# Performance work log

Measured on AMD Instinct MI355X. Metric: run time of the kernel, lower is better.

## Reference

```python
import jax, jax.numpy as jnp
import numpy as np

N_NODES = 65536
N_EDGES = 1048576
IN_DIM = 96
HID = 128
OUT = 2 * HID  # GATv2 out_channels (heads=1, concat)
N_ACT = 20
EDGE_DIM = 3
NEG_SLOPE = 0.2
LN_EPS = 1e-5


def _glorot(key, shape):
    fan_in, fan_out = shape[0], shape[1]
    lim = float(np.sqrt(6.0 / (fan_in + fan_out)))
    return jax.random.uniform(key, shape, jnp.float32, -lim, lim)


def setup_inputs() -> dict:
    key = jax.random.key(0)
    ks = jax.random.split(key, 16)
    inputs = jax.random.normal(ks[0], (N_NODES, IN_DIM), jnp.float32)
    edge_index = jax.random.randint(ks[1], (2, N_EDGES), 0, N_NODES, jnp.int32)
    edge_attr = jax.random.normal(ks[2], (N_EDGES, EDGE_DIM), jnp.float32)
    return {
        "inputs": inputs,
        "edge_index": edge_index,
        "edge_attr": edge_attr,
        # MLP base (n_layers=2, layer_norm=True)
        "W0": _glorot(ks[3], (IN_DIM, HID)), "b0": jnp.zeros((HID,), jnp.float32),
        "g0": jnp.ones((HID,), jnp.float32), "be0": jnp.zeros((HID,), jnp.float32),
        "W1": _glorot(ks[4], (HID, HID)), "b1": jnp.zeros((HID,), jnp.float32),
        "g1": jnp.ones((HID,), jnp.float32), "be1": jnp.zeros((HID,), jnp.float32),
        # GATv2Conv params (heads=1)
        "Wl": _glorot(ks[5], (HID, OUT)), "bl": jnp.zeros((OUT,), jnp.float32),
        "Wr": _glorot(ks[6], (HID, OUT)), "br": jnp.zeros((OUT,), jnp.float32),
        "We": _glorot(ks[7], (EDGE_DIM, OUT)),
        "att": _glorot(ks[8], (OUT, 1))[:, 0],
        "Wres": _glorot(ks[9], (HID, OUT)),
        "gat_bias": jnp.zeros((OUT,), jnp.float32),
        # head: ReLU -> LayerNorm(OUT) -> Linear(OUT, n_actions)
        "g2": jnp.ones((OUT,), jnp.float32), "be2": jnp.zeros((OUT,), jnp.float32),
        "Wq": _glorot(ks[10], (OUT, N_ACT)), "bq": jnp.zeros((N_ACT,), jnp.float32),
    }


def _ln(x, g, b):
    mu = jnp.mean(x, axis=-1, keepdims=True)
    var = jnp.mean(jnp.square(x - mu), axis=-1, keepdims=True)
    return (x - mu) * jax.lax.rsqrt(var + LN_EPS) * g + b


def _gatv2(x, edge_index, edge_attr, Wl, bl, Wr, br, We, att, Wres, gat_bias):
    src, dst = edge_index[0], edge_index[1]
    xl = x @ Wl + bl          # [N, OUT]  (source transform)
    xr = x @ Wr + br          # [N, OUT]  (target transform)
    ef = edge_attr @ We       # [E, OUT]
    m = xl[src] + xr[dst] + ef                      # [E, OUT]
    e = jax.nn.leaky_relu(m, NEG_SLOPE) @ att       # [E]
    # softmax over incoming edges per target node
    e_max = jax.ops.segment_max(e, dst, num_segments=N_NODES)
    ex = jnp.exp(e - e_max[dst])
    denom = jax.ops.segment_sum(ex, dst, num_segments=N_NODES)
    alpha = ex / jnp.where(denom == 0, 1.0, denom)[dst]
    out = jax.ops.segment_sum(alpha[:, None] * xl[src], dst, num_segments=N_NODES)
    return out + x @ Wres + gat_bias


def reference(inputs, edge_index, edge_attr, W0, b0, g0, be0, W1, b1, g1, be1,
              Wl, bl, Wr, br, We, att, Wres, gat_bias, g2, be2, Wq, bq):
    x = _ln(jax.nn.relu(inputs @ W0 + b0), g0, be0)
    x = _ln(jax.nn.relu(x @ W1 + b1), g1, be1)
    h = _gatv2(x, edge_index, edge_attr, Wl, bl, Wr, br, We, att, Wres, gat_bias)
    q = _ln(jax.nn.relu(h), g2, be2) @ Wq + bq
    return q
```

## Files before the change

kernel.cpp:

```cpp
#include <hip/hip_runtime.h>
#include <hip/hip_bf16.h>

#define N_NODES 65536
#define N_EDGES 1048576
#define IN_DIM 96
#define HID 128
#define OUTD 256
#define N_ACT 20

typedef unsigned short u16;
typedef unsigned char u8;
typedef unsigned int u32;
typedef __attribute__((ext_vector_type(8))) short bf16x8;
typedef __attribute__((ext_vector_type(4))) float f32x4;
typedef __attribute__((ext_vector_type(2))) float f32x2;

__device__ __forceinline__ float bf2f(u16 v) { return __uint_as_float(((u32)v) << 16); }
__device__ __forceinline__ u16 f2bf(float f) {
    u32 x = __float_as_uint(f);
    return (u16)((x + 0x7fffu + ((x >> 16) & 1u)) >> 16);
}

__device__ __forceinline__ u8 ftofp8_hw(float f) {
    return (u8)((u32)__builtin_amdgcn_cvt_pk_fp8_f32(f, f, 0, false) & 0xffu);
}

template <int CTRL>
__device__ __forceinline__ float dppadd(float p) {
    return p + __uint_as_float((u32)__builtin_amdgcn_update_dpp(
        0, (int)__float_as_uint(p), CTRL, 0xF, 0xF, true));
}
__device__ __forceinline__ float wave_sum_bcast(float p) {
    p = dppadd<0x111>(p);
    p = dppadd<0x112>(p);
    p = dppadd<0x114>(p);
    p = dppadd<0x118>(p);
    p = dppadd<0x142>(p);
    p = dppadd<0x143>(p);
    return __uint_as_float((u32)__builtin_amdgcn_readlane((int)__float_as_uint(p), 63));
}
__device__ __forceinline__ float red16(float p) {
    p = dppadd<0xB1>(p);
    p = dppadd<0x4E>(p);
    p = dppadd<0x141>(p);
    p = dppadd<0x140>(p);
    return p;
}

__global__ __launch_bounds__(256) void k_prep(
    int* __restrict__ deg,
    const float* __restrict__ Wl, const float* __restrict__ Wr, const float* __restrict__ Wres,
    u16* __restrict__ wt,
    const float* __restrict__ W0, u16* __restrict__ wt0,
    const float* __restrict__ W1, u16* __restrict__ wt1,
    const float* __restrict__ Wq, u16* __restrict__ wqB)
{
    int b = blockIdx.x, t = threadIdx.x;
    if (b < 256) {
        deg[b * 256 + t] = 0;
    } else if (b < 640) {
        int idx = (b - 256) * 256 + t;
        int nn = idx >> 7, k = idx & 127;
        float v;
        if (nn < 256) v = Wl[k * OUTD + nn];
        else if (nn < 512) v = Wr[k * OUTD + (nn - 256)];
        else v = Wres[k * OUTD + (nn - 512)];
        wt[idx] = f2bf(v);
    } else if (b < 688) {
        int idx = (b - 640) * 256 + t;
        int nn = idx / 96, k = idx - nn * 96;
        wt0[idx] = f2bf(W0[k * HID + nn]);
    } else if (b < 752) {
        int idx = (b - 688) * 256 + t;
        int nn = idx >> 7, k = idx & 127;
        wt1[idx] = f2bf(W1[k * HID + nn]);
    } else {
        int idx = (b - 752) * 256 + t;
        int tile = idx >> 12, rem = idx & 4095;
        int kk = rem >> 9, ln = (rem >> 3) & 63, j = idx & 7;
        int k = kk * 32 + (ln >> 4) * 8 + j;
        int q = tile * 16 + (ln & 15);
        wqB[idx] = (q < N_ACT) ? f2bf(Wq[k * N_ACT + q]) : (u16)0;
    }
}

__global__ __launch_bounds__(1024) void k_scan(const int* __restrict__ deg, int* __restrict__ off) {
    __shared__ int part[1024];
    int t = threadIdx.x;
    int base = t * 64;
    const int4* d4 = (const int4*)(deg + base);
    int s = 0;
#pragma unroll
    for (int i = 0; i < 16; i++) { int4 v = d4[i]; s += v.x + v.y + v.z + v.w; }
    part[t] = s;
    __syncthreads();
    for (int o = 1; o < 1024; o <<= 1) {
        int v = (t >= o) ? part[t - o] : 0;
        __syncthreads();
        part[t] += v;
        __syncthreads();
    }
    int run = (t == 0) ? 0 : part[t - 1];
    int4* o4 = (int4*)(off + base);
#pragma unroll
    for (int i = 0; i < 16; i++) {
        int4 v = d4[i];
        int4 w;
        w.x = run;
        w.y = run + v.x;
        w.z = w.y + v.y;
        w.w = w.z + v.z;
        run = w.w + v.w;
        o4[i] = w;
    }
    if (t == 1023) off[N_NODES] = run;
}

__global__ __launch_bounds__(256) void k_scatter(
    const int* __restrict__ ei, const float* __restrict__ ea,
    const int* __restrict__ off, const int* __restrict__ rank,
    int4* __restrict__ erec)
{
    int e = blockIdx.x * 256 + threadIdx.x;
    int src = ei[e];
    int dst = ei[N_EDGES + e];
    float a0 = ea[e * 3 + 0];
    float a1 = ea[e * 3 + 1];
    float a2 = ea[e * 3 + 2];
    int pos = off[dst] + rank[e];
    erec[pos] = make_int4(src, __float_as_int(a0), __float_as_int(a1), __float_as_int(a2));
}

__global__ __launch_bounds__(256, 4) void k_fused(
    const float* __restrict__ in,
    const u16* __restrict__ wt0, const u16* __restrict__ wt1, const u16* __restrict__ wt,
    const float* __restrict__ b0, const float* __restrict__ g0, const float* __restrict__ be0,
    const float* __restrict__ b1, const float* __restrict__ g1, const float* __restrict__ be1,
    const float* __restrict__ bl, const float* __restrict__ br, const float* __restrict__ gbias,
    const int* __restrict__ ei, int* __restrict__ deg, int* __restrict__ rank,
    u8* __restrict__ xl8, u16* __restrict__ xr, u16* __restrict__ hres)
{
    if (blockIdx.x >= 512) {
        int e = (blockIdx.x - 512) * 256 + threadIdx.x;
        rank[e] = atomicAdd(deg + ei[N_EDGES + e], 1);
        return;
    }
    int wid = threadIdx.x >> 6, lane = threadIdx.x & 63;
    int l15 = lane & 15, quad = lane >> 4;
    int m0 = (blockIdx.x * 4 + wid) * 32;

    __shared__ u16 xbuf[4][32][136];

    f32x4 acc[2][8];

#pragma unroll
    for (int mt = 0; mt < 2; mt++)
#pragma unroll
        for (int t = 0; t < 8; t++) acc[mt][t] = {0.f, 0.f, 0.f, 0.f};
#pragma unroll
    for (int kk = 0; kk < 3; kk++) {
        bf16x8 af[2];
#pragma unroll
        for (int mt = 0; mt < 2; mt++) {
            const float* ap = in + (long)(m0 + mt * 16 + l15) * IN_DIM + kk * 32 + quad * 8;
            float4 fa = *(const float4*)(ap);
            float4 fb = *(const float4*)(ap + 4);
            af[mt][0] = (short)f2bf(fa.x); af[mt][1] = (short)f2bf(fa.y);
            af[mt][2] = (short)f2bf(fa.z); af[mt][3] = (short)f2bf(fa.w);
            af[mt][4] = (short)f2bf(fb.x); af[mt][5] = (short)f2bf(fb.y);
            af[mt][6] = (short)f2bf(fb.z); af[mt][7] = (short)f2bf(fb.w);
        }
#pragma unroll
        for (int t = 0; t < 8; t++) {
            bf16x8 bf = *(const bf16x8*)(wt0 + (t * 16 + l15) * IN_DIM + kk * 32 + quad * 8);
            acc[0][t] = __builtin_amdgcn_mfma_f32_16x16x32_bf16(af[0], bf, acc[0][t], 0, 0, 0);
            acc[1][t] = __builtin_amdgcn_mfma_f32_16x16x32_bf16(af[1], bf, acc[1][t], 0, 0, 0);
        }
    }
    {
        float bv[8], gv[8], bev[8];
#pragma unroll
        for (int t = 0; t < 8; t++) {
            int col = t * 16 + l15;
            bv[t] = b0[col]; gv[t] = g0[col]; bev[t] = be0[col];
        }
#pragma unroll
        for (int mt = 0; mt < 2; mt++) {
#pragma unroll
            for (int g = 0; g < 4; g++) {
                float s_ = 0.f, q_ = 0.f;
#pragma unroll
                for (int t = 0; t < 8; t++) {
                    float x = fmaxf(acc[mt][t][g] + bv[t], 0.f);
                    acc[mt][t][g] = x;
                    s_ += x;
                    q_ = fmaf(x, x, q_);
                }
                s_ = red16(s_);
                q_ = red16(q_);
                float mu = s_ * (1.f / HID);
                float var = q_ * (1.f / HID) - mu * mu;
                float rs = rsqrtf(fmaxf(var, 0.f) + 1e-5f);
#pragma unroll
                for (int t = 0; t < 8; t++) {
                    float y = (acc[mt][t][g] - mu) * rs * gv[t] + bev[t];
                    xbuf[wid][mt * 16 + quad * 4 + g][t * 16 + l15] = f2bf(y);
                }
            }
        }
    }

#pragma unroll
    for (int mt = 0; mt < 2; mt++)
#pragma unroll
        for (int t = 0; t < 8; t++) acc[mt][t] = {0.f, 0.f, 0.f, 0.f};
#pragma unroll
    for (int kk = 0; kk < 4; kk++) {
        bf16x8 af0 = *(const bf16x8*)(&xbuf[wid][l15][kk * 32 + quad * 8]);
        bf16x8 af1 = *(const bf16x8*)(&xbuf[wid][16 + l15][kk * 32 + quad * 8]);
#pragma unroll
        for (int t = 0; t < 8; t++) {
            bf16x8 bf = *(const bf16x8*)(wt1 + (t * 16 + l15) * HID + kk * 32 + quad * 8);
            acc[0][t] = __builtin_amdgcn_mfma_f32_16x16x32_bf16(af0, bf, acc[0][t], 0, 0, 0);
            acc[1][t] = __builtin_amdgcn_mfma_f32_16x16x32_bf16(af1, bf, acc[1][t], 0, 0, 0);
        }
    }
    {
        float bv[8], gv[8], bev[8];
#pragma unroll
        for (int t = 0; t < 8; t++) {
            int col = t * 16 + l15;
            bv[t] = b1[col]; gv[t] = g1[col]; bev[t] = be1[col];
        }
#pragma unroll
        for (int mt = 0; mt < 2; mt++) {
#pragma unroll
            for (int g = 0; g < 4; g++) {
                float s_ = 0.f, q_ = 0.f;
#pragma unroll
                for (int t = 0; t < 8; t++) {
                    float x = fmaxf(acc[mt][t][g] + bv[t], 0.f);
                    acc[mt][t][g] = x;
                    s_ += x;
                    q_ = fmaf(x, x, q_);
                }
                s_ = red16(s_);
                q_ = red16(q_);
                float mu = s_ * (1.f / HID);
                float var = q_ * (1.f / HID) - mu * mu;
                float rs = rsqrtf(fmaxf(var, 0.f) + 1e-5f);
#pragma unroll
                for (int t = 0; t < 8; t++) {
                    float y = (acc[mt][t][g] - mu) * rs * gv[t] + bev[t];
                    xbuf[wid][mt * 16 + quad * 4 + g][t * 16 + l15] = f2bf(y);
                }
            }
        }
    }

    for (int nT = 0; nT < 3; nT++) {
        for (int h = 0; h < 2; h++) {
            f32x4 pacc[2][8];
#pragma unroll
            for (int mt = 0; mt < 2; mt++)
#pragma unroll
                for (int t = 0; t < 8; t++) pacc[mt][t] = {0.f, 0.f, 0.f, 0.f};
#pragma unroll
            for (int kk = 0; kk < 4; kk++) {
                bf16x8 af0 = *(const bf16x8*)(&xbuf[wid][l15][kk * 32 + quad * 8]);
                bf16x8 af1 = *(const bf16x8*)(&xbuf[wid][16 + l15][kk * 32 + quad * 8]);
#pragma unroll
                for (int t = 0; t < 8; t++) {
                    bf16x8 bf = *(const bf16x8*)(wt + (long)(nT * 256 + h * 128 + t * 16 + l15) * HID + kk * 32 + quad * 8);
                    pacc[0][t] = __builtin_amdgcn_mfma_f32_16x16x32_bf16(af0, bf, pacc[0][t], 0, 0, 0);
                    pacc[1][t] = __builtin_amdgcn_mfma_f32_16x16x32_bf16(af1, bf, pacc[1][t], 0, 0, 0);
                }
            }
            if (nT == 0) {
#pragma unroll
                for (int t = 0; t < 8; t++) {
                    int col = h * 128 + t * 16 + l15;
                    float bvv = bl[col];
#pragma unroll
                    for (int mt = 0; mt < 2; mt++)
#pragma unroll
                        for (int g = 0; g < 4; g++) {
                            xl8[(long)(m0 + mt * 16 + quad * 4 + g) * OUTD + col] = ftofp8_hw(pacc[mt][t][g] + bvv);
                        }
                }
            } else {
                const float* bias = (nT == 1) ? br : gbias;
                u16* dst = (nT == 1) ? xr : hres;
#pragma unroll
                for (int t = 0; t < 8; t++) {
                    int col = h * 128 + t * 16 + l15;
                    float bvv = bias[col];
#pragma unroll
                    for (int mt = 0; mt < 2; mt++)
#pragma unroll
                        for (int g = 0; g < 4; g++) {
                            dst[(long)(m0 + mt * 16 + quad * 4 + g) * OUTD + col] = f2bf(pacc[mt][t][g] + bvv);
                        }
                }
            }
        }
    }
}

__global__ __launch_bounds__(256, 4) void k_agg_fused(
    const int* __restrict__ off, const int4* __restrict__ erec,
    const u8* __restrict__ xl8, const u16* __restrict__ xr, const u16* __restrict__ hres,
    const float* __restrict__ We, const float* __restrict__ att,
    const float* __restrict__ g2, const float* __restrict__ be2,
    const u16* __restrict__ wqB, const float* __restrict__ bq,
    float* __restrict__ out)
{
    int wid = threadIdx.x >> 6, lane = threadIdx.x & 63;
    int n = blockIdx.x * 4 + wid;
    int j0 = lane * 4;
    __shared__ __align__(16) u16 ylds[4][256];

    const float LOG2E = 1.44269504088896f;

    float4 w0 = *(const float4*)(We + j0);
    float4 w1 = *(const float4*)(We + OUTD + j0);
    float4 w2 = *(const float4*)(We + 2 * OUTD + j0);
    float4 avf = *(const float4*)(att + j0);
    f32x2 w0_01 = {w0.x, w0.y}, w0_23 = {w0.z, w0.w};
    f32x2 w1_01 = {w1.x, w1.y}, w1_23 = {w1.z, w1.w};
    f32x2 w2_01 = {w2.x, w2.y}, w2_23 = {w2.z, w2.w};
    f32x2 av01 = {avf.x * LOG2E, avf.y * LOG2E};
    f32x2 av23 = {avf.z * LOG2E, avf.w * LOG2E};

    ushort4 xrv = *(const ushort4*)(xr + (long)n * OUTD + j0);
    f32x2 xr01 = {bf2f(xrv.x), bf2f(xrv.y)};
    f32x2 xr23 = {bf2f(xrv.z), bf2f(xrv.w)};

    int beg = off[n], end = off[n + 1];

    float s = 0.f;
    f32x2 a01 = {0.f, 0.f}, a23 = {0.f, 0.f};

    auto logit = [&](const int4& r, u32 v, f32x2& d0, f32x2& d1) -> float {
        d0 = __builtin_amdgcn_cvt_pk_f32_fp8((int)v, false);
        d1 = __builtin_amdgcn_cvt_pk_f32_fp8((int)v, true);
        f32x2 ea0 = {__int_as_float(r.y), __int_as_float(r.y)};
        f32x2 ea1 = {__int_as_float(r.z), __int_as_float(r.z)};
        f32x2 ea2 = {__int_as_float(r.w), __int_as_float(r.w)};
        f32x2 t01 = d0 + xr01;
        t01 = __builtin_elementwise_fma(ea0, w0_01, t01);
        t01 = __builtin_elementwise_fma(ea1, w1_01, t01);
        t01 = __builtin_elementwise_fma(ea2, w2_01, t01);
        f32x2 t23 = d1 + xr23;
        t23 = __builtin_elementwise_fma(ea0, w0_23, t23);
        t23 = __builtin_elementwise_fma(ea1, w1_23, t23);
        t23 = __builtin_elementwise_fma(ea2, w2_23, t23);
        f32x2 l01 = __builtin_elementwise_max(t01, 0.2f * t01);
        f32x2 l23 = __builtin_elementwise_max(t23, 0.2f * t23);
        f32x2 pv = l01 * av01;
        pv = __builtin_elementwise_fma(l23, av23, pv);
        return pv[0] + pv[1];
    };

    if (beg < end) {
        int4 r0, r1, r2, r3;
        u32 v0, v1, v2, v3;
        {
            int i1 = min(beg + 1, end - 1), i2 = min(beg + 2, end - 1), i3 = min(beg + 3, end - 1);
            r0 = erec[beg]; r1 = erec[i1]; r2 = erec[i2]; r3 = erec[i3];
            v0 = *(const u32*)(xl8 + (long)r0.x * OUTD + j0);
            v1 = *(const u32*)(xl8 + (long)r1.x * OUTD + j0);
            v2 = *(const u32*)(xl8 + (long)r2.x * OUTD + j0);
            v3 = *(const u32*)(xl8 + (long)r3.x * OUTD + j0);
        }
#pragma unroll 1
        for (int i = beg; i < end; i += 4) {
            int nb = i + 4;
            int p0i = min(nb, end - 1), p1i = min(nb + 1, end - 1);
            int p2i = min(nb + 2, end - 1), p3i = min(nb + 3, end - 1);
            int4 nr0 = erec[p0i], nr1 = erec[p1i], nr2 = erec[p2i], nr3 = erec[p3i];
            u32 nv0 = *(const u32*)(xl8 + (long)nr0.x * OUTD + j0);
            u32 nv1 = *(const u32*)(xl8 + (long)nr1.x * OUTD + j0);
            u32 nv2 = *(const u32*)(xl8 + (long)nr2.x * OUTD + j0);
            u32 nv3 = *(const u32*)(xl8 + (long)nr3.x * OUTD + j0);

            f32x2 d00, d01, d10, d11, d20, d21, d30, d31;
            float p0 = logit(r0, v0, d00, d01);
            float p1 = logit(r1, v1, d10, d11);
            float p2 = logit(r2, v2, d20, d21);
            float p3 = logit(r3, v3, d30, d31);

            p0 = wave_sum_bcast(p0);
            p1 = wave_sum_bcast(p1);
            p2 = wave_sum_bcast(p2);
            p3 = wave_sum_bcast(p3);
            if (i + 1 >= end) p1 = -1.0e30f;
            if (i + 2 >= end) p2 = -1.0e30f;
            if (i + 3 >= end) p3 = -1.0e30f;

            float e0 = __builtin_amdgcn_exp2f(p0);
            float e1 = __builtin_amdgcn_exp2f(p1);
            float e2 = __builtin_amdgcn_exp2f(p2);
            float e3 = __builtin_amdgcn_exp2f(p3);
            s += (e0 + e1) + (e2 + e3);

            f32x2 e0v = {e0, e0}, e1v = {e1, e1}, e2v = {e2, e2}, e3v = {e3, e3};
            a01 = __builtin_elementwise_fma(e0v, d00, a01);
            a23 = __builtin_elementwise_fma(e0v, d01, a23);
            a01 = __builtin_elementwise_fma(e1v, d10, a01);
            a23 = __builtin_elementwise_fma(e1v, d11, a23);
            a01 = __builtin_elementwise_fma(e2v, d20, a01);
            a23 = __builtin_elementwise_fma(e2v, d21, a23);
            a01 = __builtin_elementwise_fma(e3v, d30, a01);
            a23 = __builtin_elementwise_fma(e3v, d31, a23);

            r0 = nr0; r1 = nr1; r2 = nr2; r3 = nr3;
            v0 = nv0; v1 = nv1; v2 = nv2; v3 = nv3;
        }
    }

    float inv = (end > beg) ? 1.f / s : 0.f;

    ushort4 hv = *(const ushort4*)(hres + (long)n * OUTD + j0);
    float h0 = fmaxf(fmaf(a01[0], inv, bf2f(hv.x)), 0.f);
    float h1 = fmaxf(fmaf(a01[1], inv, bf2f(hv.y)), 0.f);
    float h2 = fmaxf(fmaf(a23[0], inv, bf2f(hv.z)), 0.f);
    float h3 = fmaxf(fmaf(a23[1], inv, bf2f(hv.w)), 0.f);

    float sum = h0 + h1 + h2 + h3;
    float sq = h0 * h0 + h1 * h1 + h2 * h2 + h3 * h3;
    sum = wave_sum_bcast(sum);
    sq = wave_sum_bcast(sq);
    float mu = sum * (1.f / OUTD);
    float var = sq * (1.f / OUTD) - mu * mu;
    float rs = rsqrtf(fmaxf(var, 0.f) + 1e-5f);

    float4 gv = *(const float4*)(g2 + j0);
    float4 bv = *(const float4*)(be2 + j0);
    ushort4 yy;
    yy.x = f2bf((h0 - mu) * rs * gv.x + bv.x);
    yy.y = f2bf((h1 - mu) * rs * gv.y + bv.y);
    yy.z = f2bf((h2 - mu) * rs * gv.z + bv.z);
    yy.w = f2bf((h3 - mu) * rs * gv.w + bv.w);
    *(ushort4*)(&ylds[wid][j0]) = yy;
    __syncthreads();

    if (wid < 2) {
        int row = lane & 15, qd = lane >> 4;
        const u16* ab = &ylds[row & 3][qd * 8];
        f32x4 cacc = {0.f, 0.f, 0.f, 0.f};
#pragma unroll
        for (int kk = 0; kk < 8; kk++) {
            bf16x8 afrag = *(const bf16x8*)(ab + kk * 32);
            bf16x8 bfrag = *(const bf16x8*)(wqB + ((((wid << 3) + kk) << 6) + lane) * 8);
            cacc = __builtin_amdgcn_mfma_f32_16x16x32_bf16(afrag, bfrag, cacc, 0, 0, 0);
        }
        if (lane < 16) {
            int q = wid * 16 + lane;
            if (q < N_ACT) {
                float bqv = bq[q];
                long nb = (long)blockIdx.x * 4;
#pragma unroll
                for (int g = 0; g < 4; g++)
                    out[(nb + g) * N_ACT + q] = cacc[g] + bqv;
            }
        }
    }
}

extern "C" void kernel_launch(void* const* d_in, const int* in_sizes, int n_in,
                              void* d_out, int out_size, void* d_ws, size_t ws_size,
                              hipStream_t stream) {
    (void)in_sizes; (void)n_in; (void)out_size; (void)ws_size;
    const float* inp  = (const float*)d_in[0];
    const int*   ei   = (const int*)d_in[1];
    const float* ea   = (const float*)d_in[2];
    const float* W0   = (const float*)d_in[3];
    const float* b0   = (const float*)d_in[4];
    const float* g0   = (const float*)d_in[5];
    const float* be0  = (const float*)d_in[6];
    const float* W1   = (const float*)d_in[7];
    const float* b1   = (const float*)d_in[8];
    const float* g1   = (const float*)d_in[9];
    const float* be1  = (const float*)d_in[10];
    const float* Wl   = (const float*)d_in[11];
    const float* bl   = (const float*)d_in[12];
    const float* Wr   = (const float*)d_in[13];
    const float* br   = (const float*)d_in[14];
    const float* We   = (const float*)d_in[15];
    const float* att  = (const float*)d_in[16];
    const float* Wres = (const float*)d_in[17];
    const float* gbias= (const float*)d_in[18];
    const float* g2   = (const float*)d_in[19];
    const float* be2  = (const float*)d_in[20];
    const float* Wq   = (const float*)d_in[21];
    const float* bq   = (const float*)d_in[22];
    float* out = (float*)d_out;

    char* ws = (char*)d_ws;
    size_t o = 0;
    auto alloc = [&](size_t bytes) -> void* {
        void* p = ws + o;
        o += (bytes + 255) & ~(size_t)255;
        return p;
    };
    u8*    xl8    = (u8*)   alloc((size_t)N_NODES * OUTD);
    u16*   xr     = (u16*)  alloc((size_t)N_NODES * OUTD * 2);
    u16*   hres   = (u16*)  alloc((size_t)N_NODES * OUTD * 2);
    int*   deg    = (int*)  alloc((size_t)N_NODES * 4);
    int*   off    = (int*)  alloc((size_t)(N_NODES + 1) * 4);
    int*   rank   = (int*)  alloc((size_t)N_EDGES * 4);
    int4*  erec   = (int4*) alloc((size_t)N_EDGES * 16);
    u16*   wt     = (u16*)  alloc((size_t)768 * HID * 2);
    u16*   wt0    = (u16*)  alloc((size_t)HID * IN_DIM * 2);
    u16*   wt1    = (u16*)  alloc((size_t)HID * HID * 2);
    u16*   wqB    = (u16*)  alloc((size_t)2 * 8 * 64 * 8 * 2);

    k_prep<<<784, 256, 0, stream>>>(deg, Wl, Wr, Wres, wt, W0, wt0, W1, wt1, Wq, wqB);
    k_fused<<<512 + N_EDGES / 256, 256, 0, stream>>>(inp, wt0, wt1, wt,
        b0, g0, be0, b1, g1, be1, bl, br, gbias, ei, deg, rank, xl8, xr, hres);
    k_scan<<<1, 1024, 0, stream>>>(deg, off);
    k_scatter<<<N_EDGES / 256, 256, 0, stream>>>(ei, ea, off, rank, erec);
    k_agg_fused<<<N_NODES / 4, 256, 0, stream>>>(off, erec, xl8, xr, hres, We, att, g2, be2, wqB, bq, out);
}
```

Before: 411.9 us.

## Split each wave into two half-waves processing alternate edges with 8 features per lane

The aggregation kernel now has each 32-lane half of a wave handle a different edge, with each lane covering 8 output features instead of 4. The logit reduction shrinks to a 32-lane reduction (DPP plus ds_swizzle), and the two halves' partial sums and accumulators are combined with a cross-half shuffle at the end. This is meant to cut the per-edge cross-lane reduction cost and raise memory-level parallelism through a deeper prefetch pipeline. In exchange it adds per-lane registers and merge shuffles, and it relies on the LayerNorm statistics being correctly rescaled for the duplicated halves.

```diff
diff --git a/kernel.cpp b/kernel.cpp
--- a/kernel.cpp
+++ b/kernel.cpp
@@ -44,6 +44,12 @@
     p = dppadd<0x4E>(p);
     p = dppadd<0x141>(p);
     p = dppadd<0x140>(p);
+    return p;
+}
+__device__ __forceinline__ float red32(float p) {
+    p = red16(p);
+    p = p + __uint_as_float((u32)__builtin_amdgcn_ds_swizzle(
+        (int)__float_as_uint(p), 0x401F));
     return p;
 }
 
@@ -316,133 +322,143 @@
     float* __restrict__ out)
 {
     int wid = threadIdx.x >> 6, lane = threadIdx.x & 63;
+    int half = lane >> 5, l31 = lane & 31;
     int n = blockIdx.x * 4 + wid;
-    int j0 = lane * 4;
+    int j0 = l31 * 8;
     __shared__ __align__(16) u16 ylds[4][256];
 
     const float LOG2E = 1.44269504088896f;
 
-    float4 w0 = *(const float4*)(We + j0);
-    float4 w1 = *(const float4*)(We + OUTD + j0);
-    float4 w2 = *(const float4*)(We + 2 * OUTD + j0);
-    float4 avf = *(const float4*)(att + j0);
-    f32x2 w0_01 = {w0.x, w0.y}, w0_23 = {w0.z, w0.w};
-    f32x2 w1_01 = {w1.x, w1.y}, w1_23 = {w1.z, w1.w};
-    f32x2 w2_01 = {w2.x, w2.y}, w2_23 = {w2.z, w2.w};
-    f32x2 av01 = {avf.x * LOG2E, avf.y * LOG2E};
-    f32x2 av23 = {avf.z * LOG2E, avf.w * LOG2E};
-
-    ushort4 xrv = *(const ushort4*)(xr + (long)n * OUTD + j0);
-    f32x2 xr01 = {bf2f(xrv.x), bf2f(xrv.y)};
-    f32x2 xr23 = {bf2f(xrv.z), bf2f(xrv.w)};
+    f32x2 w0_[4], w1_[4], w2_[4], at_[4], xr_[4];
+    {
+        float4 a0 = *(const float4*)(We + j0);
+        float4 a1 = *(const float4*)(We + j0 + 4);
+        w0_[0] = {a0.x, a0.y}; w0_[1] = {a0.z, a0.w}; w0_[2] = {a1.x, a1.y}; w0_[3] = {a1.z, a1.w};
+        float4 b0v = *(const float4*)(We + OUTD + j0);
+        float4 b1v = *(const float4*)(We + OUTD + j0 + 4);
+        w1_[0] = {b0v.x, b0v.y}; w1_[1] = {b0v.z, b0v.w}; w1_[2] = {b1v.x, b1v.y}; w1_[3] = {b1v.z, b1v.w};
+        float4 c0 = *(const float4*)(We + 2 * OUTD + j0);
+        float4 c1 = *(const float4*)(We + 2 * OUTD + j0 + 4);
+        w2_[0] = {c0.x, c0.y}; w2_[1] = {c0.z, c0.w}; w2_[2] = {c1.x, c1.y}; w2_[3] = {c1.z, c1.w};
+        float4 t0 = *(const float4*)(att + j0);
+        float4 t1 = *(const float4*)(att + j0 + 4);
+        at_[0] = {t0.x * LOG2E, t0.y * LOG2E}; at_[1] = {t0.z * LOG2E, t0.w * LOG2E};
+        at_[2] = {t1.x * LOG2E, t1.y * LOG2E}; at_[3] = {t1.z * LOG2E, t1.w * LOG2E};
+        ushort4 xa = *(const ushort4*)(xr + (long)n * OUTD + j0);
+        ushort4 xb = *(const ushort4*)(xr + (long)n * OUTD + j0 + 4);
+        xr_[0] = {bf2f(xa.x), bf2f(xa.y)}; xr_[1] = {bf2f(xa.z), bf2f(xa.w)};
+        xr_[2] = {bf2f(xb.x), bf2f(xb.y)}; xr_[3] = {bf2f(xb.z), bf2f(xb.w)};
+    }
 
     int beg = off[n], end = off[n + 1];
+    int cnt = end - beg;
 
     float s = 0.f;
-    f32x2 a01 = {0.f, 0.f}, a23 = {0.f, 0.f};
-
-    auto logit = [&](const int4& r, u32 v, f32x2& d0, f32x2& d1) -> float {
-        d0 = __builtin_amdgcn_cvt_pk_f32_fp8((int)v, false);
-        d1 = __builtin_amdgcn_cvt_pk_f32_fp8((int)v, true);
-        f32x2 ea0 = {__int_as_float(r.y), __int_as_float(r.y)};
-        f32x2 ea1 = {__int_as_float(r.z), __int_as_float(r.z)};
-        f32x2 ea2 = {__int_as_float(r.w), __int_as_float(r.w)};
-        f32x2 t01 = d0 + xr01;
-        t01 = __builtin_elementwise_fma(ea0, w0_01, t01);
-        t01 = __builtin_elementwise_fma(ea1, w1_01, t01);
-        t01 = __builtin_elementwise_fma(ea2, w2_01, t01);
-        f32x2 t23 = d1 + xr23;
-        t23 = __builtin_elementwise_fma(ea0, w0_23, t23);
-        t23 = __builtin_elementwise_fma(ea1, w1_23, t23);
-        t23 = __builtin_elementwise_fma(ea2, w2_23, t23);
-        f32x2 l01 = __builtin_elementwise_max(t01, 0.2f * t01);
-        f32x2 l23 = __builtin_elementwise_max(t23, 0.2f * t23);
-        f32x2 pv = l01 * av01;
-        pv = __builtin_elementwise_fma(l23, av23, pv);
-        return pv[0] + pv[1];
-    };
-
-    if (beg < end) {
-        int4 r0, r1, r2, r3;
-        u32 v0, v1, v2, v3;
-        {
-            int i1 = min(beg + 1, end - 1), i2 = min(beg + 2, end - 1), i3 = min(beg + 3, end - 1);
-            r0 = erec[beg]; r1 = erec[i1]; r2 = erec[i2]; r3 = erec[i3];
-            v0 = *(const u32*)(xl8 + (long)r0.x * OUTD + j0);
-            v1 = *(const u32*)(xl8 + (long)r1.x * OUTD + j0);
-            v2 = *(const u32*)(xl8 + (long)r2.x * OUTD + j0);
-            v3 = *(const u32*)(xl8 + (long)r3.x * OUTD + j0);
-        }
+    f32x2 a_[4] = {{0.f, 0.f}, {0.f, 0.f}, {0.f, 0.f}, {0.f, 0.f}};
+
+    if (cnt > 0) {
+        const u8* xbase = xl8 + j0;
+        auto ix = [&](int k) { return beg + min(k + half, cnt - 1); };
+        int4 R0 = erec[ix(0)];
+        int4 R1 = erec[ix(2)];
+        int4 R2 = erec[ix(4)];
+        uint2 V0 = *(const uint2*)(xbase + (long)R0.x * OUTD);
+        uint2 V1 = *(const uint2*)(xbase + (long)R1.x * OUTD);
 #pragma unroll 1
-        for (int i = beg; i < end; i += 4) {
-            int nb = i + 4;
-            int p0i = min(nb, end - 1), p1i = min(nb + 1, end - 1);
-            int p2i = min(nb + 2, end - 1), p3i = min(nb + 3, end - 1);
-            int4 nr0 = erec[p0i], nr1 = erec[p1i], nr2 = erec[p2i], nr3 = erec[p3i];
-            u32 nv0 = *(const u32*)(xl8 + (long)nr0.x * OUTD + j0);
-            u32 nv1 = *(const u32*)(xl8 + (long)nr1.x * OUTD + j0);
-            u32 nv2 = *(const u32*)(xl8 + (long)nr2.x * OUTD + j0);
-            u32 nv3 = *(const u32*)(xl8 + (long)nr3.x * OUTD + j0);
-
-            f32x2 d00, d01, d10, d11, d20, d21, d30, d31;
-            float p0 = logit(r0, v0, d00, d01);
-            float p1 = logit(r1, v1, d10, d11);
-            float p2 = logit(r2, v2, d20, d21);
-            float p3 = logit(r3, v3, d30, d31);
-
-            p0 = wave_sum_bcast(p0);
-            p1 = wave_sum_bcast(p1);
-            p2 = wave_sum_bcast(p2);
-            p3 = wave_sum_bcast(p3);
-            if (i + 1 >= end) p1 = -1.0e30f;
-            if (i + 2 >= end) p2 = -1.0e30f;
-            if (i + 3 >= end) p3 = -1.0e30f;
-
-            float e0 = __builtin_amdgcn_exp2f(p0);
-            float e1 = __builtin_amdgcn_exp2f(p1);
-            float e2 = __builtin_amdgcn_exp2f(p2);
-            float e3 = __builtin_amdgcn_exp2f(p3);
-            s += (e0 + e1) + (e2 + e3);
-
-            f32x2 e0v = {e0, e0}, e1v = {e1, e1}, e2v = {e2, e2}, e3v = {e3, e3};
-            a01 = __builtin_elementwise_fma(e0v, d00, a01);
-            a23 = __builtin_elementwise_fma(e0v, d01, a23);
-            a01 = __builtin_elementwise_fma(e1v, d10, a01);
-            a23 = __builtin_elementwise_fma(e1v, d11, a23);
-            a01 = __builtin_elementwise_fma(e2v, d20, a01);
-            a23 = __builtin_elementwise_fma(e2v, d21, a23);
-            a01 = __builtin_elementwise_fma(e3v, d30, a01);
-            a23 = __builtin_elementwise_fma(e3v, d31, a23);
-
-            r0 = nr0; r1 = nr1; r2 = nr2; r3 = nr3;
-            v0 = nv0; v1 = nv1; v2 = nv2; v3 = nv3;
-        }
-    }
-
-    float inv = (end > beg) ? 1.f / s : 0.f;
-
-    ushort4 hv = *(const ushort4*)(hres + (long)n * OUTD + j0);
-    float h0 = fmaxf(fmaf(a01[0], inv, bf2f(hv.x)), 0.f);
-    float h1 = fmaxf(fmaf(a01[1], inv, bf2f(hv.y)), 0.f);
-    float h2 = fmaxf(fmaf(a23[0], inv, bf2f(hv.z)), 0.f);
-    float h3 = fmaxf(fmaf(a23[1], inv, bf2f(hv.w)), 0.f);
-
-    float sum = h0 + h1 + h2 + h3;
-    float sq = h0 * h0 + h1 * h1 + h2 * h2 + h3 * h3;
+        for (int i = 0; i < cnt; i += 2) {
+            int4 R3 = erec[ix(i + 6)];
+            uint2 V2 = *(const uint2*)(xbase + (long)R2.x * OUTD);
+
+            f32x2 d0 = __builtin_amdgcn_cvt_pk_f32_fp8((int)V0.x, false);
+            f32x2 d1 = __builtin_amdgcn_cvt_pk_f32_fp8((int)V0.x, true);
+            f32x2 d2 = __builtin_amdgcn_cvt_pk_f32_fp8((int)V0.y, false);
+            f32x2 d3 = __builtin_amdgcn_cvt_pk_f32_fp8((int)V0.y, true);
+
+            float ea0 = __int_as_float(R0.y), ea1 = __int_as_float(R0.z), ea2 = __int_as_float(R0.w);
+            f32x2 e0v = {ea0, ea0}, e1v = {ea1, ea1}, e2v = {ea2, ea2};
+
+            f32x2 m0 = d0 + xr_[0], m1 = d1 + xr_[1], m2 = d2 + xr_[2], m3 = d3 + xr_[3];
+            m0 = __builtin_elementwise_fma(e0v, w0_[0], m0);
+            m1 = __builtin_elementwise_fma(e0v, w0_[1], m1);
+            m2 = __builtin_elementwise_fma(e0v, w0_[2], m2);
+            m3 = __builtin_elementwise_fma(e0v, w0_[3], m3);
+            m0 = __builtin_elementwise_fma(e1v, w1_[0], m0);
+            m1 = __builtin_elementwise_fma(e1v, w1_[1], m1);
+            m2 = __builtin_elementwise_fma(e1v, w1_[2], m2);
+            m3 = __builtin_elementwise_fma(e1v, w1_[3], m3);
+            m0 = __builtin_elementwise_fma(e2v, w2_[0], m0);
+            m1 = __builtin_elementwise_fma(e2v, w2_[1], m1);
+            m2 = __builtin_elementwise_fma(e2v, w2_[2], m2);
+            m3 = __builtin_elementwise_fma(e2v, w2_[3], m3);
+            m0 = __builtin_elementwise_max(m0, 0.2f * m0);
+            m1 = __builtin_elementwise_max(m1, 0.2f * m1);
+            m2 = __builtin_elementwise_max(m2, 0.2f * m2);
+            m3 = __builtin_elementwise_max(m3, 0.2f * m3);
+
+            f32x2 pv = m0 * at_[0];
+            pv = __builtin_elementwise_fma(m1, at_[1], pv);
+            pv = __builtin_elementwise_fma(m2, at_[2], pv);
+            pv = __builtin_elementwise_fma(m3, at_[3], pv);
+            float p = pv[0] + pv[1];
+
+            p = red32(p);
+            if (i + half >= cnt) p = -1.0e30f;
+            float e = __builtin_amdgcn_exp2f(p);
+            s += e;
+
+            f32x2 ev = {e, e};
+            a_[0] = __builtin_elementwise_fma(ev, d0, a_[0]);
+            a_[1] = __builtin_elementwise_fma(ev, d1, a_[1]);
+            a_[2] = __builtin_elementwise_fma(ev, d2, a_[2]);
+            a_[3] = __builtin_elementwise_fma(ev, d3, a_[3]);
+
+            R0 = R1; R1 = R2; R2 = R3;
+            V0 = V1; V1 = V2;
+        }
+        s += __shfl_xor(s, 32);
+#pragma unroll
+        for (int k = 0; k < 4; k++) {
+            a_[k][0] += __shfl_xor(a_[k][0], 32);
+            a_[k][1] += __shfl_xor(a_[k][1], 32);
+        }
+    }
+
+    float inv = (cnt > 0) ? 1.f / s : 0.f;
+
+    ushort4 ha = *(const ushort4*)(hres + (long)n * OUTD + j0);
+    ushort4 hb = *(const ushort4*)(hres + (long)n * OUTD + j0 + 4);
+    float h[8];
+    h[0] = fmaxf(fmaf(a_[0][0], inv, bf2f(ha.x)), 0.f);
+    h[1] = fmaxf(fmaf(a_[0][1], inv, bf2f(ha.y)), 0.f);
+    h[2] = fmaxf(fmaf(a_[1][0], inv, bf2f(ha.z)), 0.f);
+    h[3] = fmaxf(fmaf(a_[1][1], inv, bf2f(ha.w)), 0.f);
+    h[4] = fmaxf(fmaf(a_[2][0], inv, bf2f(hb.x)), 0.f);
+    h[5] = fmaxf(fmaf(a_[2][1], inv, bf2f(hb.y)), 0.f);
+    h[6] = fmaxf(fmaf(a_[3][0], inv, bf2f(hb.z)), 0.f);
+    h[7] = fmaxf(fmaf(a_[3][1], inv, bf2f(hb.w)), 0.f);
+
+    float sum = ((h[0] + h[1]) + (h[2] + h[3])) + ((h[4] + h[5]) + (h[6] + h[7]));
+    float sq = 0.f;
+#pragma unroll
+    for (int k = 0; k < 8; k++) sq = fmaf(h[k], h[k], sq);
     sum = wave_sum_bcast(sum);
     sq = wave_sum_bcast(sq);
-    float mu = sum * (1.f / OUTD);
-    float var = sq * (1.f / OUTD) - mu * mu;
+    float mu = sum * (1.f / (2 * OUTD));
+    float var = sq * (1.f / (2 * OUTD)) - mu * mu;
     float rs = rsqrtf(fmaxf(var, 0.f) + 1e-5f);
 
-    float4 gv = *(const float4*)(g2 + j0);
-    float4 bv = *(const float4*)(be2 + j0);
-    ushort4 yy;
-    yy.x = f2bf((h0 - mu) * rs * gv.x + bv.x);
-    yy.y = f2bf((h1 - mu) * rs * gv.y + bv.y);
-    yy.z = f2bf((h2 - mu) * rs * gv.z + bv.z);
-    yy.w = f2bf((h3 - mu) * rs * gv.w + bv.w);
-    *(ushort4*)(&ylds[wid][j0]) = yy;
+    {
+        int jw = j0 + half * 4;
+        float4 gv = *(const float4*)(g2 + jw);
+        float4 bv = *(const float4*)(be2 + jw);
+        int o0 = half * 4;
+        ushort4 yy;
+        yy.x = f2bf((h[o0 + 0] - mu) * rs * gv.x + bv.x);
+        yy.y = f2bf((h[o0 + 1] - mu) * rs * gv.y + bv.y);
+        yy.z = f2bf((h[o0 + 2] - mu) * rs * gv.z + bv.z);
+        yy.w = f2bf((h[o0 + 3] - mu) * rs * gv.w + bv.w);
+        *(ushort4*)(&ylds[wid][jw]) = yy;
+    }
     __syncthreads();
 
     if (wid < 2) {
```

After: 414.8 us. No clear change (+0.7%).
